# Kernel tuning notes

Hardware: AMD Instinct MI355X
Metric: run time of the kernel (lower is better)

## Reference

```python
import jax, jax.numpy as jnp
import numpy as np

N = 50000        # nodes
E = 800000       # edges (avg degree 16)
F_IN = 128
H = 128
C = 16


def setup_inputs() -> dict:
    key = jax.random.key(0)
    ks = jax.random.split(key, 12)
    x = jax.random.normal(ks[0], (N, F_IN), dtype=jnp.float32)
    edges = jax.random.randint(ks[1], (2, E), 0, N, dtype=jnp.int32)
    dims = [(F_IN, H), (H, H // 2), (H // 2, H // 4), (H // 4, H // 8), (H // 8, C)]
    params = {}
    for i, (di, do) in enumerate(dims):
        params[f"W{i+1}"] = jax.random.normal(ks[2 + 2 * i], (di, do), dtype=jnp.float32) * (1.0 / np.sqrt(di)).astype(np.float32)
        params[f"b{i+1}"] = jax.random.normal(ks[3 + 2 * i], (do,), dtype=jnp.float32) * 0.01
    return {"x": x, "edges": edges, **params}


def reference(x, edges, W1, b1, W2, b2, W3, b3, W4, b4, W5, b5):
    src, dst = edges[0], edges[1]
    ones = jnp.ones((E,), x.dtype)
    # symmetric ('both') normalization with degree clamped to >= 1 (DGL GraphConv default)
    out_deg = jnp.clip(jax.ops.segment_sum(ones, src, num_segments=N), 1.0, None)
    in_deg = jnp.clip(jax.ops.segment_sum(ones, dst, num_segments=N), 1.0, None)
    norm_src = (out_deg ** -0.5)[:, None]   # [N,1]
    norm_dst = (in_deg ** -0.5)[:, None]    # [N,1]

    def graph_conv(h, W, b):
        h = h @ W                                  # dense transform first (out <= in)
        msgs = (h * norm_src)[src]                 # [E, d_out] gather
        agg = jax.ops.segment_sum(msgs, dst, num_segments=N)  # scatter-add SpMM
        return agg * norm_dst + b

    h = x
    for W, b in ((W1, b1), (W2, b2), (W3, b3), (W4, b4), (W5, b5)):
        h = jax.nn.relu(graph_conv(h, W, b))
    return h
```

## Files before the change

kernel.cpp:

```cpp
#include <hip/hip_runtime.h>
#include <hip/hip_bf16.h>


#define THREADS 256
#define HIST_B 256
#define HWORDS 12500
#define RS_BLOCKS 49

typedef __attribute__((ext_vector_type(8))) short short8_t;
typedef __attribute__((ext_vector_type(4))) float float4_t;

__device__ __forceinline__ unsigned short f2bf_rne(float f) {
    unsigned u = __builtin_bit_cast(unsigned, f);
    unsigned r = u + 0x7fffu + ((u >> 16) & 1u);
    return (unsigned short)(r >> 16);
}
__device__ __forceinline__ float bf2f(unsigned short h) {
    return __builtin_bit_cast(float, ((unsigned)h) << 16);
}

template<int K, int NOUT, bool NORM>
__device__ __forceinline__ void gemm_core(const float* __restrict__ A,
                                          const short* lh, const short* ll,
                                          const float* __restrict__ norm,
                                          short* __restrict__ outq,
                                          float* __restrict__ qscale,
                                          int M, int blk, int tid) {
    constexpr int Kp  = (K + 31) & ~31;
    constexpr int STR = Kp + 8;
    constexpr int NT  = NOUT / 16;

    const int w    = tid >> 6;
    const int lane = tid & 63;
    const int ln   = lane & 15;
    const int quad = lane >> 4;
    const int row  = blk * 64 + w * 16 + ln;
    const bool rv  = row < M;

    float4_t acc[NT];
#pragma unroll
    for (int i = 0; i < NT; ++i) acc[i] = (float4_t){0.f, 0.f, 0.f, 0.f};

#pragma unroll
    for (int kt = 0; kt < Kp / 32; ++kt) {
        const int k0 = kt * 32 + quad * 8;
        float a[8];
        if (rv && k0 < K) {
            float4 v0 = *(const float4*)&A[(size_t)row * K + k0];
            float4 v1 = *(const float4*)&A[(size_t)row * K + k0 + 4];
            a[0] = v0.x; a[1] = v0.y; a[2] = v0.z; a[3] = v0.w;
            a[4] = v1.x; a[5] = v1.y; a[6] = v1.z; a[7] = v1.w;
        } else {
#pragma unroll
            for (int j = 0; j < 8; ++j) a[j] = 0.f;
        }
        short8_t ahi, alo;
#pragma unroll
        for (int j = 0; j < 8; ++j) {
            unsigned short h = f2bf_rne(a[j]);
            ahi[j] = (short)h;
            alo[j] = (short)f2bf_rne(a[j] - bf2f(h));
        }
#pragma unroll
        for (int nt = 0; nt < NT; ++nt) {
            const int bidx = (nt * 16 + ln) * STR + kt * 32 + quad * 8;
            short8_t bh = *(const short8_t*)&lh[bidx];
            short8_t bl = *(const short8_t*)&ll[bidx];
            acc[nt] = __builtin_amdgcn_mfma_f32_16x16x32_bf16(ahi, bh, acc[nt], 0, 0, 0);
            acc[nt] = __builtin_amdgcn_mfma_f32_16x16x32_bf16(ahi, bl, acc[nt], 0, 0, 0);
            acc[nt] = __builtin_amdgcn_mfma_f32_16x16x32_bf16(alo, bh, acc[nt], 0, 0, 0);
        }
    }

    const int orow = blk * 64 + w * 16 + quad * 4;
#pragma unroll
    for (int i = 0; i < 4; ++i) {
        int r = orow + i;
        float m = 0.f;
#pragma unroll
        for (int nt = 0; nt < NT; ++nt) m = fmaxf(m, fabsf(acc[nt][i]));
#pragma unroll
        for (int off = 1; off < 16; off <<= 1) m = fmaxf(m, __shfl_xor(m, off));
        float s = 1.f;
        if (NORM) s = (r < M) ? norm[r] : 0.f;
        float rowmax = m * s;
        float inv = (rowmax > 0.f) ? (32767.f / rowmax) : 0.f;
        if (r < M) {
            if (ln == 0) qscale[r] = rowmax * (1.f / 32767.f);
#pragma unroll
            for (int nt = 0; nt < NT; ++nt)
                outq[(size_t)r * NOUT + nt * 16 + ln] =
                    (short)(int)__builtin_rintf(acc[nt][i] * s * inv);
        }
    }
}

__device__ __forceinline__ void conv_one(const float* __restrict__ W, short* __restrict__ hi,
                                         short* __restrict__ lo, int K, int NOUT, int STR, int i) {
    int n = i / STR;
    int kk = i % STR;
    float v = (kk < K) ? W[(size_t)kk * NOUT + n] : 0.f;
    unsigned short h = f2bf_rne(v);
    hi[i] = (short)h;
    lo[i] = (short)f2bf_rne(v - bf2f(h));
}

__global__ __launch_bounds__(THREADS)
void packed0_kernel(const float* __restrict__ x, const float* __restrict__ W1,
                    const float* __restrict__ W2, const float* __restrict__ W3,
                    const float* __restrict__ W4, const float* __restrict__ W5,
                    short* __restrict__ tq, float* __restrict__ qscale,
                    const int* __restrict__ src, const int* __restrict__ dst,
                    unsigned* __restrict__ p_src, unsigned* __restrict__ p_dst,
                    unsigned char* __restrict__ rank, int* __restrict__ flags,
                    short* w2h, short* w2l, short* w3h, short* w3l,
                    short* w4h, short* w4l, short* w5h, short* w5l,
                    int E, int chunk, int N, int G1) {
    __shared__ __align__(16) char smem[69632];
    const int blk = blockIdx.x;
    const int t = threadIdx.x;

    if (blk < G1) {
        short* lh = (short*)smem;
        short* ll = (short*)smem + 17408;
        for (int j = t; j < 128 * 128; j += THREADS) {
            int kk = j >> 7, n = j & 127;
            float v = W1[j];
            unsigned short h = f2bf_rne(v);
            lh[n * 136 + kk] = (short)h;
            ll[n * 136 + kk] = (short)f2bf_rne(v - bf2f(h));
        }
        __syncthreads();
        gemm_core<128, 128, false>(x, lh, ll, nullptr, tq, qscale, N, blk, t);
    } else if (blk < G1 + 2 * HIST_B) {
        unsigned* bins = (unsigned*)smem;
        const int hb = blk - G1;
        const bool is_dst = hb < HIST_B;
        const int b = is_dst ? hb : hb - HIST_B;
        const int e0 = b * chunk;
        int e1 = e0 + chunk; if (e1 > E) e1 = E;
        const int* __restrict__ idx = is_dst ? dst : src;
        unsigned* __restrict__ pout = is_dst ? p_dst : p_src;

        for (int w = t; w < HWORDS; w += THREADS) bins[w] = 0;
        __syncthreads();
        for (int e = e0 + t; e < e1; e += THREADS) {
            int d = idx[e];
            unsigned sh = (unsigned)(d & 3) * 8u;
            unsigned old = atomicAdd(&bins[d >> 2], 1u << sh);
            if (is_dst) rank[e] = (unsigned char)((old >> sh) & 0xffu);
        }
        __syncthreads();
        for (int w = t; w < HWORDS; w += THREADS)
            pout[(size_t)b * HWORDS + w] = bins[w];
    } else {
        int cb = blk - G1 - 2 * HIST_B;
        if (cb == 48) {
            if (t < 64) flags[t] = 0;
            return;
        }
        int i = cb * THREADS + t;
        if (i < 8704)                        conv_one(W2, w2h, w2l, 128, 64, 136, i);
        else if ((i -= 8704) < 2304)         conv_one(W3, w3h, w3l, 64, 32, 72, i);
        else if ((i -= 2304) < 640)          conv_one(W4, w4h, w4l, 32, 16, 40, i);
        else { i -= 640;                     conv_one(W5, w5h, w5l, 16, 16, 40, i); }
    }
}

__global__ __launch_bounds__(THREADS)
void reduce_scan_kernel(const unsigned* __restrict__ p_src, unsigned* __restrict__ p_dst,
                        float* __restrict__ norm_src, float* __restrict__ norm_dst,
                        float* __restrict__ qscale, int* __restrict__ row_ptr,
                        int* __restrict__ flags, int N) {
    __shared__ int sh[THREADS];
    __shared__ int bexcl_sh;
    const int t = threadIdx.x;
    const int b = blockIdx.x;
    const int w = b * THREADS + t;

    int d0 = 0, d1 = 0, d2 = 0, d3 = 0;
    if (w < HWORDS) {
        unsigned s = 0;
#pragma unroll 4
        for (int c = 0; c < HIST_B; ++c) s += p_src[(size_t)c * HWORDS + w];

        unsigned run = 0;
#pragma unroll 4
        for (int c = 0; c < HIST_B; ++c) {
            size_t i = (size_t)c * HWORDS + w;
            unsigned v = p_dst[i];
            p_dst[i] = run;
            run += v;
        }
        d0 = (int)(run & 0xffu); d1 = (int)((run >> 8) & 0xffu);
        d2 = (int)((run >> 16) & 0xffu); d3 = (int)(run >> 24);

#pragma unroll
        for (int l = 0; l < 4; ++l) {
            int node = 4 * w + l;
            if (node < N) {
                int dd = (l == 0) ? d0 : (l == 1) ? d1 : (l == 2) ? d2 : d3;
                int ds = (int)((s >> (8 * l)) & 0xffu);
                norm_dst[node] = rsqrtf((float)(dd < 1 ? 1 : dd));
                float ns = rsqrtf((float)(ds < 1 ? 1 : ds));
                norm_src[node] = ns;
                qscale[node] *= ns;
            }
        }
    }

    int tsum = d0 + d1 + d2 + d3;
    sh[t] = tsum;
    __syncthreads();
#pragma unroll
    for (int off = 1; off < THREADS; off <<= 1) {
        int u = 0;
        if (t >= off) u = sh[t - off];
        __syncthreads();
        sh[t] += u;
        __syncthreads();
    }
    const int btotal = sh[THREADS - 1];
    const int lexcl  = sh[t] - tsum;

    if (t == 0) atomicExch(&flags[b], btotal + 1);
    if (t < 64) {
        int v = 0;
        if (t < b) {
            int f;
            do { f = atomicAdd(&flags[t], 0); } while (f == 0);
            v = f - 1;
        }
#pragma unroll
        for (int off = 1; off < 64; off <<= 1) v += __shfl_xor(v, off);
        if (t == 0) bexcl_sh = v;
    }
    __syncthreads();

    int pre = bexcl_sh + lexcl;
    int n0 = 4 * w;
    if (n0 + 0 < N) row_ptr[n0 + 0] = pre; pre += d0;
    if (n0 + 1 < N) row_ptr[n0 + 1] = pre; pre += d1;
    if (n0 + 2 < N) row_ptr[n0 + 2] = pre; pre += d2;
    if (n0 + 3 < N) row_ptr[n0 + 3] = pre;
    if (b == RS_BLOCKS - 1 && t == THREADS - 1) row_ptr[N] = bexcl_sh + btotal;
}

__global__ __launch_bounds__(THREADS)
void scatter_kernel(const int* __restrict__ src, const int* __restrict__ dst,
                    const unsigned char* __restrict__ rank,
                    const int* __restrict__ row_ptr, const unsigned* __restrict__ p_dst,
                    int* __restrict__ col, int E, int chunk) {
    const int b = blockIdx.x;
    const int e0 = b * chunk;
    int e1 = e0 + chunk; if (e1 > E) e1 = E;
    for (int e = e0 + threadIdx.x; e < e1; e += THREADS) {
        int d = dst[e];
        unsigned sh = (unsigned)(d & 3) * 8u;
        unsigned pre = (p_dst[(size_t)b * HWORDS + (d >> 2)] >> sh) & 0xffu;
        col[row_ptr[d] + (int)pre + (int)rank[e]] = src[e];
    }
}

template<int K, int NOUT>
__global__ __launch_bounds__(THREADS)
void gemm_mfma_kernel(const float* __restrict__ A, const short* __restrict__ wt_hi,
                      const short* __restrict__ wt_lo, const float* __restrict__ norm,
                      short* __restrict__ outq, float* __restrict__ qscale, int M) {
    constexpr int Kp  = (K + 31) & ~31;
    constexpr int STR = Kp + 8;

    __shared__ short lh[NOUT * STR];
    __shared__ short ll[NOUT * STR];

    const int tid = threadIdx.x;
    {
        constexpr int CNT = NOUT * STR / 2;
        const int* gh = (const int*)wt_hi;
        const int* gl = (const int*)wt_lo;
        int* sh = (int*)lh;
        int* sl = (int*)ll;
        for (int i = tid; i < CNT; i += THREADS) { sh[i] = gh[i]; sl[i] = gl[i]; }
    }
    __syncthreads();
    gemm_core<K, NOUT, true>(A, lh, ll, norm, outq, qscale, M, blockIdx.x, tid);
}

template<int D>
__global__ __launch_bounds__(THREADS)
void agg_q_kernel(const short* __restrict__ tq, const float* __restrict__ qscale,
                  const int* __restrict__ row_ptr, const int* __restrict__ col,
                  const float* __restrict__ norm_dst, const float* __restrict__ bias,
                  float* __restrict__ out, int N) {
    constexpr int TPN = D / 8;
    constexpr int NPB = THREADS / TPN;
    const int tid  = threadIdx.x;
    const int ln   = tid % TPN;
    const int g    = tid / TPN;
    const int node = blockIdx.x * NPB + g;
    if (node >= N) return;

    const int beg = row_ptr[node];
    const int end = row_ptr[node + 1];

    float acc[8];
#pragma unroll
    for (int c = 0; c < 8; ++c) acc[c] = 0.f;

    int j = beg;
    for (; j + 3 < end; j += 4) {
        int s0 = col[j], s1 = col[j + 1], s2 = col[j + 2], s3 = col[j + 3];
        short8_t v0 = *(const short8_t*)&tq[(size_t)s0 * D + ln * 8];
        short8_t v1 = *(const short8_t*)&tq[(size_t)s1 * D + ln * 8];
        short8_t v2 = *(const short8_t*)&tq[(size_t)s2 * D + ln * 8];
        short8_t v3 = *(const short8_t*)&tq[(size_t)s3 * D + ln * 8];
        float c0 = qscale[s0], c1 = qscale[s1], c2 = qscale[s2], c3 = qscale[s3];
#pragma unroll
        for (int c = 0; c < 8; ++c)
            acc[c] += (float)v0[c] * c0 + (float)v1[c] * c1
                    + (float)v2[c] * c2 + (float)v3[c] * c3;
    }
    for (; j < end; ++j) {
        int s0 = col[j];
        short8_t v0 = *(const short8_t*)&tq[(size_t)s0 * D + ln * 8];
        float c0 = qscale[s0];
#pragma unroll
        for (int c = 0; c < 8; ++c) acc[c] += (float)v0[c] * c0;
    }

    float nd = norm_dst[node];
    float4 b0 = *(const float4*)&bias[ln * 8];
    float4 b1 = *(const float4*)&bias[ln * 8 + 4];
    float4 o0, o1;
    o0.x = fmaxf(acc[0] * nd + b0.x, 0.f);
    o0.y = fmaxf(acc[1] * nd + b0.y, 0.f);
    o0.z = fmaxf(acc[2] * nd + b0.z, 0.f);
    o0.w = fmaxf(acc[3] * nd + b0.w, 0.f);
    o1.x = fmaxf(acc[4] * nd + b1.x, 0.f);
    o1.y = fmaxf(acc[5] * nd + b1.y, 0.f);
    o1.z = fmaxf(acc[6] * nd + b1.z, 0.f);
    o1.w = fmaxf(acc[7] * nd + b1.w, 0.f);
    *(float4*)&out[(size_t)node * D + ln * 8] = o0;
    *(float4*)&out[(size_t)node * D + ln * 8 + 4] = o1;
}

extern "C" void kernel_launch(void* const* d_in, const int* in_sizes, int n_in,
                              void* d_out, int out_size, void* d_ws, size_t ws_size,
                              hipStream_t stream) {
    const float* x     = (const float*)d_in[0];
    const int*   edges = (const int*)d_in[1];
    const float* W1 = (const float*)d_in[2];  const float* b1 = (const float*)d_in[3];
    const float* W2 = (const float*)d_in[4];  const float* b2 = (const float*)d_in[5];
    const float* W3 = (const float*)d_in[6];  const float* b3 = (const float*)d_in[7];
    const float* W4 = (const float*)d_in[8];  const float* b4 = (const float*)d_in[9];
    const float* W5 = (const float*)d_in[10]; const float* b5 = (const float*)d_in[11];

    const int N = in_sizes[0] / 128;
    const int E = in_sizes[1] / 2;
    const int* src = edges;
    const int* dst = edges + E;

    char* ws = (char*)d_ws;
    size_t off = 0;
    auto carve = [&](size_t bytes) -> void* {
        void* p = ws + off;
        off += (bytes + 255) & ~(size_t)255;
        return p;
    };
    short* tq       = (short*)carve((size_t)N * 128 * 2);
    float* hbuf     = (float*)carve((size_t)N * 128 * 4);
    float* norm_src = (float*)carve((size_t)N * 4);
    float* norm_dst = (float*)carve((size_t)N * 4);
    int*   row_ptr  = (int*)carve((size_t)(N + 1) * 4);
    int*   col      = (int*)carve((size_t)E * 4);
    float* qscale   = (float*)carve((size_t)N * 4);
    int*   flags    = (int*)carve((size_t)64 * 4);
    short* wts      = (short*)carve((size_t)24576 * 2);
    unsigned* p_src = (unsigned*)carve((size_t)HIST_B * HWORDS * 4);
    unsigned* p_dst = (unsigned*)carve((size_t)HIST_B * HWORDS * 4);
    unsigned char* rank = (unsigned char*)carve((size_t)E);
    (void)ws_size;

    short* w2h = wts;            short* w2l = w2h + 8704;
    short* w3h = w2l + 8704;     short* w3l = w3h + 2304;
    short* w4h = w3l + 2304;     short* w4l = w4h + 640;
    short* w5h = w4l + 640;      short* w5l = w5h + 640;

    const int chunk = (E + HIST_B - 1) / HIST_B;
    const int gridG = (N + 63) / 64;

    packed0_kernel<<<gridG + 2 * HIST_B + RS_BLOCKS, THREADS, 0, stream>>>(
        x, W1, W2, W3, W4, W5, tq, qscale, src, dst, p_src, p_dst, rank, flags,
        w2h, w2l, w3h, w3l, w4h, w4l, w5h, w5l, E, chunk, N, gridG);

    reduce_scan_kernel<<<RS_BLOCKS, THREADS, 0, stream>>>(
        p_src, p_dst, norm_src, norm_dst, qscale, row_ptr, flags, N);

    scatter_kernel<<<HIST_B, THREADS, 0, stream>>>(src, dst, rank, row_ptr, p_dst, col, E, chunk);

    agg_q_kernel<128><<<(N + 15) / 16, THREADS, 0, stream>>>(tq, qscale, row_ptr, col, norm_dst, b1, hbuf, N);

    gemm_mfma_kernel<128, 64><<<gridG, THREADS, 0, stream>>>(hbuf, w2h, w2l, norm_src, tq, qscale, N);
    agg_q_kernel<64><<<(N + 31) / 32, THREADS, 0, stream>>>(tq, qscale, row_ptr, col, norm_dst, b2, hbuf, N);

    gemm_mfma_kernel<64, 32><<<gridG, THREADS, 0, stream>>>(hbuf, w3h, w3l, norm_src, tq, qscale, N);
    agg_q_kernel<32><<<(N + 63) / 64, THREADS, 0, stream>>>(tq, qscale, row_ptr, col, norm_dst, b3, hbuf, N);

    gemm_mfma_kernel<32, 16><<<gridG, THREADS, 0, stream>>>(hbuf, w4h, w4l, norm_src, tq, qscale, N);
    agg_q_kernel<16><<<(N + 127) / 128, THREADS, 0, stream>>>(tq, qscale, row_ptr, col, norm_dst, b4, hbuf, N);

    gemm_mfma_kernel<16, 16><<<gridG, THREADS, 0, stream>>>(hbuf, w5h, w5l, norm_src, tq, qscale, N);
    agg_q_kernel<16><<<(N + 127) / 128, THREADS, 0, stream>>>(tq, qscale, row_ptr, col, norm_dst, b5, (float*)d_out, N);
}
```

Before: 296.7 us.

## Split layer-1 GEMM into column halves and widen reduce-scan and scatter grids

Layer-1 GEMM blocks now each compute 64 of the 128 output columns, which doubles the block count and roughly halves shared memory per block. Each half gets its own quantisation scale, so qscale becomes two entries per node and the first aggregation reads the scale matching its column half. The reduce/scan kernel goes from 49 to 196 blocks, with four quarter-waves each summing 64 histogram chunks in registers. The scatter kernel now runs with twice as many blocks. The aim is more parallelism in the front-end stages, at the cost of rereading x twice, more cross-block flag polling in the scan, and changed per-half quantisation numerics.

New measurement: 278.8 us. 1.06x faster.

```diff
diff --git a/kernel.cpp b/kernel.cpp
--- a/kernel.cpp
+++ b/kernel.cpp
@@ -5,7 +5,8 @@
 #define THREADS 256
 #define HIST_B 256
 #define HWORDS 12500
-#define RS_BLOCKS 49
+#define RS_BLOCKS 196
+#define G1BLKS 1564
 
 typedef __attribute__((ext_vector_type(8))) short short8_t;
 typedef __attribute__((ext_vector_type(4))) float float4_t;
@@ -25,7 +26,9 @@
                                           const float* __restrict__ norm,
                                           short* __restrict__ outq,
                                           float* __restrict__ qscale,
-                                          int M, int blk, int tid) {
+                                          int M, int blk, int tid,
+                                          int ostride, int ocol0,
+                                          int qstride, int qoff) {
     constexpr int Kp  = (K + 31) & ~31;
     constexpr int STR = Kp + 8;
     constexpr int NT  = NOUT / 16;
@@ -86,10 +89,10 @@
         float rowmax = m * s;
         float inv = (rowmax > 0.f) ? (32767.f / rowmax) : 0.f;
         if (r < M) {
-            if (ln == 0) qscale[r] = rowmax * (1.f / 32767.f);
+            if (ln == 0) qscale[r * qstride + qoff] = rowmax * (1.f / 32767.f);
 #pragma unroll
             for (int nt = 0; nt < NT; ++nt)
-                outq[(size_t)r * NOUT + nt * 16 + ln] =
+                outq[(size_t)r * ostride + ocol0 + nt * 16 + ln] =
                     (short)(int)__builtin_rintf(acc[nt][i] * s * inv);
         }
     }
@@ -109,32 +112,35 @@
 void packed0_kernel(const float* __restrict__ x, const float* __restrict__ W1,
                     const float* __restrict__ W2, const float* __restrict__ W3,
                     const float* __restrict__ W4, const float* __restrict__ W5,
-                    short* __restrict__ tq, float* __restrict__ qscale,
+                    short* __restrict__ tq, float* __restrict__ qscale2,
                     const int* __restrict__ src, const int* __restrict__ dst,
                     unsigned* __restrict__ p_src, unsigned* __restrict__ p_dst,
                     unsigned char* __restrict__ rank, int* __restrict__ flags,
                     short* w2h, short* w2l, short* w3h, short* w3l,
                     short* w4h, short* w4l, short* w5h, short* w5l,
-                    int E, int chunk, int N, int G1) {
-    __shared__ __align__(16) char smem[69632];
+                    int E, int chunk, int N) {
+    __shared__ __align__(16) char smem[50048];
     const int blk = blockIdx.x;
     const int t = threadIdx.x;
 
-    if (blk < G1) {
+    if (blk < G1BLKS) {
+        const int h  = blk & 1;
+        const int gb = blk >> 1;
         short* lh = (short*)smem;
-        short* ll = (short*)smem + 17408;
-        for (int j = t; j < 128 * 128; j += THREADS) {
-            int kk = j >> 7, n = j & 127;
-            float v = W1[j];
-            unsigned short h = f2bf_rne(v);
-            lh[n * 136 + kk] = (short)h;
-            ll[n * 136 + kk] = (short)f2bf_rne(v - bf2f(h));
+        short* ll = (short*)smem + 8704;
+        for (int j = t; j < 128 * 64; j += THREADS) {
+            int kk = j >> 6, n = j & 63;
+            float v = W1[kk * 128 + h * 64 + n];
+            unsigned short hh = f2bf_rne(v);
+            lh[n * 136 + kk] = (short)hh;
+            ll[n * 136 + kk] = (short)f2bf_rne(v - bf2f(hh));
         }
         __syncthreads();
-        gemm_core<128, 128, false>(x, lh, ll, nullptr, tq, qscale, N, blk, t);
-    } else if (blk < G1 + 2 * HIST_B) {
+        gemm_core<128, 64, false>(x, lh, ll, nullptr, tq, qscale2, N, gb, t,
+                                  128, h * 64, 2, h);
+    } else if (blk < G1BLKS + 2 * HIST_B) {
         unsigned* bins = (unsigned*)smem;
-        const int hb = blk - G1;
+        const int hb = blk - G1BLKS;
         const bool is_dst = hb < HIST_B;
         const int b = is_dst ? hb : hb - HIST_B;
         const int e0 = b * chunk;
@@ -154,9 +160,9 @@
         for (int w = t; w < HWORDS; w += THREADS)
             pout[(size_t)b * HWORDS + w] = bins[w];
     } else {
-        int cb = blk - G1 - 2 * HIST_B;
+        int cb = blk - G1BLKS - 2 * HIST_B;
         if (cb == 48) {
-            if (t < 64) flags[t] = 0;
+            flags[t] = 0;
             return;
         }
         int i = cb * THREADS + t;
@@ -170,80 +176,110 @@
 __global__ __launch_bounds__(THREADS)
 void reduce_scan_kernel(const unsigned* __restrict__ p_src, unsigned* __restrict__ p_dst,
                         float* __restrict__ norm_src, float* __restrict__ norm_dst,
-                        float* __restrict__ qscale, int* __restrict__ row_ptr,
+                        float* __restrict__ qscale2, int* __restrict__ row_ptr,
                         int* __restrict__ flags, int N) {
-    __shared__ int sh[THREADS];
+    __shared__ unsigned qd[4][64];
+    __shared__ unsigned qs[4][64];
+    __shared__ int sscan[64];
     __shared__ int bexcl_sh;
-    const int t = threadIdx.x;
-    const int b = blockIdx.x;
-    const int w = b * THREADS + t;
-
-    int d0 = 0, d1 = 0, d2 = 0, d3 = 0;
-    if (w < HWORDS) {
-        unsigned s = 0;
-#pragma unroll 4
-        for (int c = 0; c < HIST_B; ++c) s += p_src[(size_t)c * HWORDS + w];
-
-        unsigned run = 0;
-#pragma unroll 4
-        for (int c = 0; c < HIST_B; ++c) {
-            size_t i = (size_t)c * HWORDS + w;
-            unsigned v = p_dst[i];
-            p_dst[i] = run;
-            run += v;
-        }
-        d0 = (int)(run & 0xffu); d1 = (int)((run >> 8) & 0xffu);
-        d2 = (int)((run >> 16) & 0xffu); d3 = (int)(run >> 24);
-
-#pragma unroll
-        for (int l = 0; l < 4; ++l) {
-            int node = 4 * w + l;
-            if (node < N) {
+    const int t  = threadIdx.x;
+    const int b  = blockIdx.x;
+    const int q  = t >> 6;
+    const int wl = t & 63;
+    const int w  = b * 64 + wl;
+    const bool wv = (w < HWORDS);
+
+    unsigned vals[64];
+    unsigned dsum = 0, ssum = 0;
+    if (wv) {
+#pragma unroll
+        for (int i = 0; i < 64; ++i) {
+            int c = q * 64 + i;
+            vals[i] = p_dst[(size_t)c * HWORDS + w];
+            dsum += vals[i];
+        }
+#pragma unroll
+        for (int i = 0; i < 64; ++i) {
+            int c = q * 64 + i;
+            ssum += p_src[(size_t)c * HWORDS + w];
+        }
+    }
+    qd[q][wl] = dsum;
+    qs[q][wl] = ssum;
+    __syncthreads();
+
+    unsigned off = 0, dfull = 0, sfull = 0;
+#pragma unroll
+    for (int qq = 0; qq < 4; ++qq) {
+        unsigned v = qd[qq][wl];
+        if (qq < q) off += v;
+        dfull += v;
+        sfull += qs[qq][wl];
+    }
+
+    if (wv) {
+        unsigned run = off;
+#pragma unroll
+        for (int i = 0; i < 64; ++i) {
+            int c = q * 64 + i;
+            p_dst[(size_t)c * HWORDS + w] = run;
+            run += vals[i];
+        }
+    }
+
+    int d0 = 0, d1 = 0, d2 = 0, d3 = 0, wdeg = 0;
+    if (q == 0) {
+        d0 = (int)(dfull & 0xffu); d1 = (int)((dfull >> 8) & 0xffu);
+        d2 = (int)((dfull >> 16) & 0xffu); d3 = (int)(dfull >> 24);
+        wdeg = d0 + d1 + d2 + d3;
+        if (wv) {
+#pragma unroll
+            for (int l = 0; l < 4; ++l) {
+                int node = 4 * w + l;
                 int dd = (l == 0) ? d0 : (l == 1) ? d1 : (l == 2) ? d2 : d3;
-                int ds = (int)((s >> (8 * l)) & 0xffu);
+                int ds = (int)((sfull >> (8 * l)) & 0xffu);
                 norm_dst[node] = rsqrtf((float)(dd < 1 ? 1 : dd));
                 float ns = rsqrtf((float)(ds < 1 ? 1 : ds));
                 norm_src[node] = ns;
-                qscale[node] *= ns;
+                qscale2[2 * node]     *= ns;
+                qscale2[2 * node + 1] *= ns;
             }
         }
-    }
-
-    int tsum = d0 + d1 + d2 + d3;
-    sh[t] = tsum;
+        sscan[wl] = wv ? wdeg : 0;
+    }
     __syncthreads();
-#pragma unroll
-    for (int off = 1; off < THREADS; off <<= 1) {
+    for (int o = 1; o < 64; o <<= 1) {
         int u = 0;
-        if (t >= off) u = sh[t - off];
+        if (t < 64 && t >= o) u = sscan[t - o];
         __syncthreads();
-        sh[t] += u;
+        if (t < 64) sscan[t] += u;
         __syncthreads();
     }
-    const int btotal = sh[THREADS - 1];
-    const int lexcl  = sh[t] - tsum;
+    const int btotal = sscan[63];
 
     if (t == 0) atomicExch(&flags[b], btotal + 1);
     if (t < 64) {
         int v = 0;
-        if (t < b) {
+        for (int p = t; p < b; p += 64) {
             int f;
-            do { f = atomicAdd(&flags[t], 0); } while (f == 0);
-            v = f - 1;
-        }
-#pragma unroll
-        for (int off = 1; off < 64; off <<= 1) v += __shfl_xor(v, off);
+            do { f = atomicAdd(&flags[p], 0); } while (f == 0);
+            v += f - 1;
+        }
+#pragma unroll
+        for (int o = 1; o < 64; o <<= 1) v += __shfl_xor(v, o);
         if (t == 0) bexcl_sh = v;
     }
     __syncthreads();
 
-    int pre = bexcl_sh + lexcl;
-    int n0 = 4 * w;
-    if (n0 + 0 < N) row_ptr[n0 + 0] = pre; pre += d0;
-    if (n0 + 1 < N) row_ptr[n0 + 1] = pre; pre += d1;
-    if (n0 + 2 < N) row_ptr[n0 + 2] = pre; pre += d2;
-    if (n0 + 3 < N) row_ptr[n0 + 3] = pre;
-    if (b == RS_BLOCKS - 1 && t == THREADS - 1) row_ptr[N] = bexcl_sh + btotal;
+    if (q == 0 && wv) {
+        int pre = bexcl_sh + sscan[wl] - wdeg;
+        int n0 = 4 * w;
+        row_ptr[n0 + 0] = pre; pre += d0;
+        row_ptr[n0 + 1] = pre; pre += d1;
+        row_ptr[n0 + 2] = pre; pre += d2;
+        row_ptr[n0 + 3] = pre;
+    }
+    if (b == RS_BLOCKS - 1 && t == 0) row_ptr[N] = bexcl_sh + btotal;
 }
 
 __global__ __launch_bounds__(THREADS)
@@ -251,13 +287,16 @@
                     const unsigned char* __restrict__ rank,
                     const int* __restrict__ row_ptr, const unsigned* __restrict__ p_dst,
                     int* __restrict__ col, int E, int chunk) {
-    const int b = blockIdx.x;
-    const int e0 = b * chunk;
+    const int bc = blockIdx.x >> 1;
+    const int hch = (chunk + 1) >> 1;
+    const int e0 = bc * chunk;
     int e1 = e0 + chunk; if (e1 > E) e1 = E;
-    for (int e = e0 + threadIdx.x; e < e1; e += THREADS) {
+    int s = e0 + (blockIdx.x & 1) * hch;
+    int send = s + hch; if (send > e1) send = e1;
+    for (int e = s + threadIdx.x; e < send; e += THREADS) {
         int d = dst[e];
         unsigned sh = (unsigned)(d & 3) * 8u;
-        unsigned pre = (p_dst[(size_t)b * HWORDS + (d >> 2)] >> sh) & 0xffu;
+        unsigned pre = (p_dst[(size_t)bc * HWORDS + (d >> 2)] >> sh) & 0xffu;
         col[row_ptr[d] + (int)pre + (int)rank[e]] = src[e];
     }
 }
@@ -283,10 +322,11 @@
         for (int i = tid; i < CNT; i += THREADS) { sh[i] = gh[i]; sl[i] = gl[i]; }
     }
     __syncthreads();
-    gemm_core<K, NOUT, true>(A, lh, ll, norm, outq, qscale, M, blockIdx.x, tid);
-}
-
-template<int D>
+    gemm_core<K, NOUT, true>(A, lh, ll, norm, outq, qscale, M, blockIdx.x, tid,
+                             NOUT, 0, 1, 0);
+}
+
+template<int D, bool QS2>
 __global__ __launch_bounds__(THREADS)
 void agg_q_kernel(const short* __restrict__ tq, const float* __restrict__ qscale,
                   const int* __restrict__ row_ptr, const int* __restrict__ col,
@@ -300,12 +340,17 @@
     const int node = blockIdx.x * NPB + g;
     if (node >= N) return;
 
+    const int half = QS2 ? (ln >> 3) : 0;
     const int beg = row_ptr[node];
     const int end = row_ptr[node + 1];
 
     float acc[8];
 #pragma unroll
     for (int c = 0; c < 8; ++c) acc[c] = 0.f;
+
+    auto scl = [&](int s) -> float {
+        return QS2 ? qscale[2 * s + half] : qscale[s];
+    };
 
     int j = beg;
     for (; j + 3 < end; j += 4) {
@@ -314,7 +359,7 @@
         short8_t v1 = *(const short8_t*)&tq[(size_t)s1 * D + ln * 8];
         short8_t v2 = *(const short8_t*)&tq[(size_t)s2 * D + ln * 8];
         short8_t v3 = *(const short8_t*)&tq[(size_t)s3 * D + ln * 8];
-        float c0 = qscale[s0], c1 = qscale[s1], c2 = qscale[s2], c3 = qscale[s3];
+        float c0 = scl(s0), c1 = scl(s1), c2 = scl(s2), c3 = scl(s3);
 #pragma unroll
         for (int c = 0; c < 8; ++c)
             acc[c] += (float)v0[c] * c0 + (float)v1[c] * c1
@@ -323,7 +368,7 @@
     for (; j < end; ++j) {
         int s0 = col[j];
         short8_t v0 = *(const short8_t*)&tq[(size_t)s0 * D + ln * 8];
-        float c0 = qscale[s0];
+        float c0 = scl(s0);
 #pragma unroll
         for (int c = 0; c < 8; ++c) acc[c] += (float)v0[c] * c0;
     }
@@ -373,8 +418,8 @@
     float* norm_dst = (float*)carve((size_t)N * 4);
     int*   row_ptr  = (int*)carve((size_t)(N + 1) * 4);
     int*   col      = (int*)carve((size_t)E * 4);
-    float* qscale   = (float*)carve((size_t)N * 4);
-    int*   flags    = (int*)carve((size_t)64 * 4);
+    float* qscale   = (float*)carve((size_t)2 * N * 4);
+    int*   flags    = (int*)carve((size_t)256 * 4);
     short* wts      = (short*)carve((size_t)24576 * 2);
     unsigned* p_src = (unsigned*)carve((size_t)HIST_B * HWORDS * 4);
     unsigned* p_dst = (unsigned*)carve((size_t)HIST_B * HWORDS * 4);
@@ -389,26 +434,26 @@
     const int chunk = (E + HIST_B - 1) / HIST_B;
     const int gridG = (N + 63) / 64;
 
-    packed0_kernel<<<gridG + 2 * HIST_B + RS_BLOCKS, THREADS, 0, stream>>>(
+    packed0_kernel<<<G1BLKS + 2 * HIST_B + 49, THREADS, 0, stream>>>(
         x, W1, W2, W3, W4, W5, tq, qscale, src, dst, p_src, p_dst, rank, flags,
-        w2h, w2l, w3h, w3l, w4h, w4l, w5h, w5l, E, chunk, N, gridG);
+        w2h, w2l, w3h, w3l, w4h, w4l, w5h, w5l, E, chunk, N);
 
     reduce_scan_kernel<<<RS_BLOCKS, THREADS, 0, stream>>>(
         p_src, p_dst, norm_src, norm_dst, qscale, row_ptr, flags, N);
 
-    scatter_kernel<<<HIST_B, THREADS, 0, stream>>>(src, dst, rank, row_ptr, p_dst, col, E, chunk);
-
-    agg_q_kernel<128><<<(N + 15) / 16, THREADS, 0, stream>>>(tq, qscale, row_ptr, col, norm_dst, b1, hbuf, N);
+    scatter_kernel<<<2 * HIST_B, THREADS, 0, stream>>>(src, dst, rank, row_ptr, p_dst, col, E, chunk);
+
+    agg_q_kernel<128, true><<<(N + 15) / 16, THREADS, 0, stream>>>(tq, qscale, row_ptr, col, norm_dst, b1, hbuf, N);
 
     gemm_mfma_kernel<128, 64><<<gridG, THREADS, 0, stream>>>(hbuf, w2h, w2l, norm_src, tq, qscale, N);
-    agg_q_kernel<64><<<(N + 31) / 32, THREADS, 0, stream>>>(tq, qscale, row_ptr, col, norm_dst, b2, hbuf, N);
+    agg_q_kernel<64, false><<<(N + 31) / 32, THREADS, 0, stream>>>(tq, qscale, row_ptr, col, norm_dst, b2, hbuf, N);
 
     gemm_mfma_kernel<64, 32><<<gridG, THREADS, 0, stream>>>(hbuf, w3h, w3l, norm_src, tq, qscale, N);
-    agg_q_kernel<32><<<(N + 63) / 64, THREADS, 0, stream>>>(tq, qscale, row_ptr, col, norm_dst, b3, hbuf, N);
+    agg_q_kernel<32, false><<<(N + 63) / 64, THREADS, 0, stream>>>(tq, qscale, row_ptr, col, norm_dst, b3, hbuf, N);
 
     gemm_mfma_kernel<32, 16><<<gridG, THREADS, 0, stream>>>(hbuf, w4h, w4l, norm_src, tq, qscale, N);
-    agg_q_kernel<16><<<(N + 127) / 128, THREADS, 0, stream>>>(tq, qscale, row_ptr, col, norm_dst, b4, hbuf, N);
+    agg_q_kernel<16, false><<<(N + 127) / 128, THREADS, 0, stream>>>(tq, qscale, row_ptr, col, norm_dst, b4, hbuf, N);
 
     gemm_mfma_kernel<16, 16><<<gridG, THREADS, 0, stream>>>(hbuf, w5h, w5l, norm_src, tq, qscale, N);
-    agg_q_kernel<16><<<(N + 127) / 128, THREADS, 0, stream>>>(tq, qscale, row_ptr, col, norm_dst, b5, (float*)d_out, N);
-}
+    agg_q_kernel<16, false><<<(N + 127) / 128, THREADS, 0, stream>>>(tq, qscale, row_ptr, col, norm_dst, b5, (float*)d_out, N);
+}
```
